# Optimization experiments

Measured on AMD Instinct MI355X. Metric: run time of the kernel, lower is better.

Reference implementation:

```python
import jax, jax.numpy as jnp
import numpy as np
import math

B, L, HID = 2, 2048, 1024
H, DK, RATIO, SHARED, TOPK = 4, 64, 4, 1, 2
EXP_V = 2
DV = DK * EXP_V
KEY_DIM = H * DK
VAL_DIM = KEY_DIM * EXP_V
HE = H * RATIO
KS = 4
EPS = 1e-5


def _silu(x):
    return x * jax.nn.sigmoid(x)


def _dwconv_causal(x, w):
    # x: (B, L, C), w: (C, KS); causal depthwise short conv
    xp = jnp.pad(x, ((0, 0), (KS - 1, 0), (0, 0))).transpose(0, 2, 1)
    y = jax.lax.conv_general_dilated(xp, w[:, None, :], (1,), 'VALID',
                                     feature_group_count=w.shape[0],
                                     dimension_numbers=('NCH', 'OIH', 'NCH'))
    return y.transpose(0, 2, 1)


def _l2norm(x):
    return x * jax.lax.rsqrt(jnp.sum(x * x, -1, keepdims=True) + 1e-6)


def _forward(hidden_states, Wq, Wk, Wv, Wb, Wa, Wg, Wo, conv_q, conv_k, conv_v,
             Wq_exp, Wk_exp, W_gate, A_log, dt_bias, norm_w):
    x = hidden_states
    q = _silu(_dwconv_causal(x @ Wq.T, conv_q)).reshape(B, L, H, DK)
    k = _silu(_dwconv_causal(x @ Wk.T, conv_k)).reshape(B, L, H, DK)
    v = _silu(_dwconv_causal(x @ Wv.T, conv_v)).reshape(B, L, H, DV)
    # per-head expert expansion -> (B,L,H,RATIO,DK)
    qe = jnp.einsum('blhd,hkd->blhk', q, Wq_exp).reshape(B, L, H, RATIO, DK)
    ke = jnp.einsum('blhd,hkd->blhk', k, Wk_exp).reshape(B, L, H, RATIO, DK)
    qe = _l2norm(qe) * (DK ** -0.5)
    ke = _l2norm(ke)
    # token-policy top-k routing over non-shared experts
    logits = jnp.einsum('blhd,nd->blhn', q, W_gate)
    scores = jax.nn.softmax(logits.astype(jnp.float32), axis=-1)
    tw, ti = jax.lax.top_k(scores, TOPK)
    tw = tw / jnp.sum(tw, -1, keepdims=True)
    full = jnp.sum(jax.nn.one_hot(ti + SHARED, RATIO, dtype=tw.dtype) * tw[..., None], axis=-2)
    full = full.at[..., :SHARED].set(1.0 / SHARED)
    w_r = (full / jnp.sum(full, -1, keepdims=True)).astype(x.dtype)  # (B,L,H,RATIO)
    mask = (w_r > 0).astype(x.dtype)
    beta = jax.nn.sigmoid(x @ Wb.T).reshape(B, L, H, RATIO) * mask
    g = -jnp.exp(A_log).reshape(H, RATIO) * jax.nn.softplus((x @ Wa.T) + dt_bias).reshape(B, L, H, RATIO)
    g = g * mask  # unrouted memories: exp(0)=1, no decay, no update
    # gated delta-rule recurrence over HE = H*RATIO memories
    qs = qe.reshape(B, L, HE, DK).transpose(1, 0, 2, 3)
    ks_ = ke.reshape(B, L, HE, DK).transpose(1, 0, 2, 3)
    vs = jnp.broadcast_to(v[:, :, :, None, :], (B, L, H, RATIO, DV)).reshape(B, L, HE, DV).transpose(1, 0, 2, 3)
    bs = beta.reshape(B, L, HE).transpose(1, 0, 2)
    gs = g.reshape(B, L, HE).transpose(1, 0, 2)

    def step(S, xs):
        qt, kt, vt, bt, gt = xs
        S = S * jnp.exp(gt)[..., None, None]
        kv = jnp.einsum('bhk,bhkv->bhv', kt, S)
        S = S + jnp.einsum('bhk,bhv->bhkv', kt, (vt - kv) * bt[..., None])
        return S, jnp.einsum('bhk,bhkv->bhv', qt, S)

    S0 = jnp.zeros((B, HE, DK, DV), x.dtype)
    _, o = jax.lax.scan(step, S0, (qs, ks_, vs, bs, gs))
    o = o.transpose(1, 0, 2, 3).reshape(B, L, H, RATIO, DV)
    o = jnp.einsum('blhe,blhev->blhv', w_r, o)
    # FusedRMSNormSwishGate + output projection
    gate = (x @ Wg.T).reshape(B, L, H, DV)
    o = o * jax.lax.rsqrt(jnp.mean(o * o, -1, keepdims=True) + EPS) * norm_w * _silu(gate)
    return o.reshape(B, L, VAL_DIM) @ Wo.T


def setup_inputs():
    keys = jax.random.split(jax.random.key(0), 18)
    n = lambda i, shp, sc=1.0: jax.random.normal(keys[i], shp, jnp.float32) * sc
    A = jax.random.uniform(keys[14], (HE,), jnp.float32, 1e-3, 16.0)
    dt = jnp.exp(jax.random.uniform(keys[15], (HE,), jnp.float32) * (math.log(0.1) - math.log(0.001)) + math.log(0.001))
    dt = jnp.clip(dt, 1e-4, None)
    return {
        'hidden_states': n(0, (B, L, HID)),
        'Wq': n(1, (KEY_DIM, HID), HID ** -0.5),
        'Wk': n(2, (KEY_DIM, HID), HID ** -0.5),
        'Wv': n(3, (VAL_DIM, HID), HID ** -0.5),
        'Wb': n(4, (HE, HID), HID ** -0.5),
        'Wa': n(5, (HE, HID), HID ** -0.5),
        'Wg': n(6, (VAL_DIM, HID), HID ** -0.5),
        'Wo': n(7, (HID, VAL_DIM), VAL_DIM ** -0.5),
        'conv_q': n(8, (KEY_DIM, KS), 0.5),
        'conv_k': n(9, (KEY_DIM, KS), 0.5),
        'conv_v': n(10, (VAL_DIM, KS), 0.5),
        'Wq_exp': n(11, (H, RATIO * DK, DK), DK ** -0.5),
        'Wk_exp': n(12, (H, RATIO * DK, DK), DK ** -0.5),
        'W_gate': n(13, (RATIO - SHARED, DK), DK ** -0.5),
        'A_log': jnp.log(A),
        'dt_bias': dt + jnp.log(-jnp.expm1(-dt)),
        'norm_w': jnp.ones((DV,), jnp.float32),
    }


def reference(hidden_states, Wq, Wk, Wv, Wb, Wa, Wg, Wo, conv_q, conv_k, conv_v,
              Wq_exp, Wk_exp, W_gate, A_log, dt_bias, norm_w):
    return _forward(hidden_states, Wq, Wk, Wv, Wb, Wa, Wg, Wo, conv_q, conv_k, conv_v,
                    Wq_exp, Wk_exp, W_gate, A_log, dt_bias, norm_w)
```

## Files before the change

### kernel.cpp

```cpp
#include <hip/hip_runtime.h>
#include <hip/hip_bf16.h>
#include <math.h>

#define B_    2
#define L_    2048
#define HID_  1024
#define H_    4
#define DK_   64
#define RATIO_ 4
#define HE_   16
#define DV_   128
#define T_    64
#define NC_   32
#define SPITCH 72
#define APITCH 68
#define NCAT  1408

typedef __attribute__((ext_vector_type(8))) short short8;
typedef __attribute__((ext_vector_type(4))) float f32x4;

__device__ __forceinline__ float sigmoidf_(float x){ return 1.f/(1.f+expf(-x)); }
__device__ __forceinline__ ushort f2bf(float x){
  __hip_bfloat16 h = __float2bfloat16(x);
  return *reinterpret_cast<ushort*>(&h);
}
__device__ __forceinline__ float bf2f(ushort u){
  union { uint32_t i; float f; } v; v.i = ((uint32_t)u) << 16; return v.f;
}
__device__ __forceinline__ void unpk8(uint4 w, float* f){
  f[0]=bf2f((ushort)(w.x&0xffff)); f[1]=bf2f((ushort)(w.x>>16));
  f[2]=bf2f((ushort)(w.y&0xffff)); f[3]=bf2f((ushort)(w.y>>16));
  f[4]=bf2f((ushort)(w.z&0xffff)); f[5]=bf2f((ushort)(w.z>>16));
  f[6]=bf2f((ushort)(w.w&0xffff)); f[7]=bf2f((ushort)(w.w>>16));
}

__global__ __launch_bounds__(256) void cast_bf16(const float* __restrict__ in,
                                                 ushort* __restrict__ out, int n)
{
  int i = blockIdx.x*256 + threadIdx.x;
  if (i < n) out[i] = f2bf(in[i]);
}

__global__ __launch_bounds__(256) void concat_wcat(const float* __restrict__ Wk,
    const float* __restrict__ Wv, const float* __restrict__ Wg,
    const float* __restrict__ Wb, const float* __restrict__ Wa,
    ushort* __restrict__ Wcat)
{
  int idx = blockIdx.x*256 + threadIdx.x;
  if (idx >= NCAT*1024) return;
  int r = idx >> 10, cc = idx & 1023;
  float v = 0.f;
  if      (r < 256)  v = Wk[(size_t)r*1024 + cc];
  else if (r < 768)  v = Wv[(size_t)(r-256)*1024 + cc];
  else if (r < 1280) v = Wg[(size_t)(r-768)*1024 + cc];
  else if (r < 1296) v = Wb[(size_t)(r-1280)*1024 + cc];
  else if (r < 1312) v = Wa[(size_t)(r-1296)*1024 + cc];
  Wcat[idx] = f2bf(v);
}

__global__ __launch_bounds__(256) void gemm_bf16(
    const ushort* __restrict__ A, int lda,
    const ushort* __restrict__ Bm, int ldb,
    float* __restrict__ C, int ldc, int K)
{
  __shared__ ushort As[128*32];
  __shared__ ushort Bs[128*32];
  const int tid  = threadIdx.x;
  const int wave = tid >> 6, lane = tid & 63;
  const int row0 = blockIdx.y*128, col0 = blockIdx.x*128;
  const int wr = (wave >> 1) * 64, wc = (wave & 1) * 64;
  const int frow = lane & 15;
  const int fko  = (lane >> 4) << 3;
  f32x4 acc[4][4];
  #pragma unroll
  for (int i=0;i<4;i++)
    #pragma unroll
    for (int j=0;j<4;j++) acc[i][j] = (f32x4){0.f,0.f,0.f,0.f};
  for (int k0 = 0; k0 < K; k0 += 32) {
    #pragma unroll
    for (int cc = 0; cc < 2; cc++) {
      int c  = wave*128 + cc*64 + lane;
      int r  = c >> 2;
      int ko = (c & 3) << 3;
      __builtin_amdgcn_global_load_lds(
        (const __attribute__((address_space(1))) void*)(A + (size_t)(row0+r)*lda + k0 + ko),
        (__attribute__((address_space(3))) void*)(As + (size_t)(wave*128 + cc*64)*8),
        16, 0, 0);
      __builtin_amdgcn_global_load_lds(
        (const __attribute__((address_space(1))) void*)(Bm + (size_t)(col0+r)*ldb + k0 + ko),
        (__attribute__((address_space(3))) void*)(Bs + (size_t)(wave*128 + cc*64)*8),
        16, 0, 0);
    }
    __syncthreads();
    short8 af[4], bfv[4];
    #pragma unroll
    for (int mi=0;mi<4;mi++)
      af[mi] = *reinterpret_cast<const short8*>(&As[(wr + mi*16 + frow)*32 + fko]);
    #pragma unroll
    for (int ni=0;ni<4;ni++)
      bfv[ni] = *reinterpret_cast<const short8*>(&Bs[(wc + ni*16 + frow)*32 + fko]);
    #pragma unroll
    for (int mi=0;mi<4;mi++)
      #pragma unroll
      for (int ni=0;ni<4;ni++)
        acc[mi][ni] = __builtin_amdgcn_mfma_f32_16x16x32_bf16(af[mi], bfv[ni], acc[mi][ni], 0, 0, 0);
    __syncthreads();
  }
  const int ocol = lane & 15;
  const int orow = (lane >> 4) << 2;
  #pragma unroll
  for (int mi=0;mi<4;mi++)
    #pragma unroll
    for (int ni=0;ni<4;ni++) {
      size_t base = (size_t)(row0 + wr + mi*16 + orow)*ldc + (col0 + wc + ni*16 + ocol);
      #pragma unroll
      for (int q=0;q<4;q++) C[base + (size_t)q*ldc] = acc[mi][ni][q];
    }
}

__global__ __launch_bounds__(256) void gemm_expand_bf16(
    const ushort* __restrict__ qc_bf, const ushort* __restrict__ kc_bf,
    const ushort* __restrict__ Wqeb, const ushort* __restrict__ Wkeb,
    ushort* __restrict__ qeb, ushort* __restrict__ keb)
{
  const int z = blockIdx.z;
  const int hh = z & 3;
  const ushort* A  = (z < 4 ? qc_bf : kc_bf) + hh*64;
  const ushort* Bm = (z < 4 ? Wqeb  : Wkeb ) + (size_t)hh*16384;
  ushort* C        = (z < 4 ? qeb   : keb  ) + hh*256;
  const int lda = 256, ldb = 64, ldc = 1024, K = 64;
  __shared__ ushort As[128*32];
  __shared__ ushort Bs[128*32];
  const int tid  = threadIdx.x;
  const int wave = tid >> 6, lane = tid & 63;
  const int row0 = blockIdx.y*128, col0 = blockIdx.x*128;
  const int wr = (wave >> 1) * 64, wc = (wave & 1) * 64;
  const int frow = lane & 15;
  const int fko  = (lane >> 4) << 3;
  f32x4 acc[4][4];
  #pragma unroll
  for (int i=0;i<4;i++)
    #pragma unroll
    for (int j=0;j<4;j++) acc[i][j] = (f32x4){0.f,0.f,0.f,0.f};
  for (int k0 = 0; k0 < K; k0 += 32) {
    #pragma unroll
    for (int cc = 0; cc < 2; cc++) {
      int c  = wave*128 + cc*64 + lane;
      int r  = c >> 2;
      int ko = (c & 3) << 3;
      __builtin_amdgcn_global_load_lds(
        (const __attribute__((address_space(1))) void*)(A + (size_t)(row0+r)*lda + k0 + ko),
        (__attribute__((address_space(3))) void*)(As + (size_t)(wave*128 + cc*64)*8),
        16, 0, 0);
      __builtin_amdgcn_global_load_lds(
        (const __attribute__((address_space(1))) void*)(Bm + (size_t)(col0+r)*ldb + k0 + ko),
        (__attribute__((address_space(3))) void*)(Bs + (size_t)(wave*128 + cc*64)*8),
        16, 0, 0);
    }
    __syncthreads();
    short8 af[4], bfv[4];
    #pragma unroll
    for (int mi=0;mi<4;mi++)
      af[mi] = *reinterpret_cast<const short8*>(&As[(wr + mi*16 + frow)*32 + fko]);
    #pragma unroll
    for (int ni=0;ni<4;ni++)
      bfv[ni] = *reinterpret_cast<const short8*>(&Bs[(wc + ni*16 + frow)*32 + fko]);
    #pragma unroll
    for (int mi=0;mi<4;mi++)
      #pragma unroll
      for (int ni=0;ni<4;ni++)
        acc[mi][ni] = __builtin_amdgcn_mfma_f32_16x16x32_bf16(af[mi], bfv[ni], acc[mi][ni], 0, 0, 0);
    __syncthreads();
  }
  const int ocol = lane & 15;
  const int orow = (lane >> 4) << 2;
  #pragma unroll
  for (int mi=0;mi<4;mi++)
    #pragma unroll
    for (int ni=0;ni<4;ni++) {
      size_t base = (size_t)(row0 + wr + mi*16 + orow)*ldc + (col0 + wc + ni*16 + ocol);
      #pragma unroll
      for (int q=0;q<4;q++) C[base + (size_t)q*ldc] = f2bf(acc[mi][ni][q]);
    }
}

__global__ __launch_bounds__(256) void gemm_f32_db(const float* __restrict__ A, int lda,
    const float* __restrict__ Bm, int ldb, float* __restrict__ C, int ldc,
    int M, int N, int K)
{
  __shared__ float As[2][32][64];
  __shared__ float Bs[2][32][64];
  const int tid = threadIdx.x;
  const int row0 = blockIdx.y * 64;
  const int col0 = blockIdx.x * 64;
  const int tx = tid & 15, ty = tid >> 4;
  const int r0s = tid >> 3;
  const int k4s = (tid & 7) << 2;
  float4 av0, av1, bv0, bv1;

  av0 = *(const float4*)&A[(size_t)(row0 + r0s)*lda + k4s];
  av1 = *(const float4*)&A[(size_t)(row0 + r0s + 32)*lda + k4s];
  bv0 = (col0 + r0s < N) ? *(const float4*)&Bm[(size_t)(col0 + r0s)*ldb + k4s] : make_float4(0,0,0,0);
  bv1 = (col0 + r0s + 32 < N) ? *(const float4*)&Bm[(size_t)(col0 + r0s + 32)*ldb + k4s] : make_float4(0,0,0,0);
  As[0][k4s+0][r0s] = av0.x; As[0][k4s+1][r0s] = av0.y; As[0][k4s+2][r0s] = av0.z; As[0][k4s+3][r0s] = av0.w;
  As[0][k4s+0][r0s+32] = av1.x; As[0][k4s+1][r0s+32] = av1.y; As[0][k4s+2][r0s+32] = av1.z; As[0][k4s+3][r0s+32] = av1.w;
  Bs[0][k4s+0][r0s] = bv0.x; Bs[0][k4s+1][r0s] = bv0.y; Bs[0][k4s+2][r0s] = bv0.z; Bs[0][k4s+3][r0s] = bv0.w;
  Bs[0][k4s+0][r0s+32] = bv1.x; Bs[0][k4s+1][r0s+32] = bv1.y; Bs[0][k4s+2][r0s+32] = bv1.z; Bs[0][k4s+3][r0s+32] = bv1.w;
  __syncthreads();

  float acc[4][4] = {};
  const int nt = K >> 5;
  for (int kt = 0; kt < nt; ++kt) {
    const int p = kt & 1;
    if (kt + 1 < nt) {
      int k0 = (kt+1) << 5;
      av0 = *(const float4*)&A[(size_t)(row0 + r0s)*lda + k0 + k4s];
      av1 = *(const float4*)&A[(size_t)(row0 + r0s + 32)*lda + k0 + k4s];
      bv0 = (col0 + r0s < N) ? *(const float4*)&Bm[(size_t)(col0 + r0s)*ldb + k0 + k4s] : make_float4(0,0,0,0);
      bv1 = (col0 + r0s + 32 < N) ? *(const float4*)&Bm[(size_t)(col0 + r0s + 32)*ldb + k0 + k4s] : make_float4(0,0,0,0);
    }
    #pragma unroll
    for (int kk = 0; kk < 32; kk++) {
      float4 a4 = *(const float4*)&As[p][kk][ty*4];
      float4 b4 = *(const float4*)&Bs[p][kk][tx*4];
      float a[4] = {a4.x,a4.y,a4.z,a4.w};
      float b[4] = {b4.x,b4.y,b4.z,b4.w};
      #pragma unroll
      for (int i=0;i<4;i++)
        #pragma unroll
        for (int j=0;j<4;j++) acc[i][j] += a[i]*b[j];
    }
    if (kt + 1 < nt) {
      const int q = p ^ 1;
      As[q][k4s+0][r0s] = av0.x; As[q][k4s+1][r0s] = av0.y; As[q][k4s+2][r0s] = av0.z; As[q][k4s+3][r0s] = av0.w;
      As[q][k4s+0][r0s+32] = av1.x; As[q][k4s+1][r0s+32] = av1.y; As[q][k4s+2][r0s+32] = av1.z; As[q][k4s+3][r0s+32] = av1.w;
      Bs[q][k4s+0][r0s] = bv0.x; Bs[q][k4s+1][r0s] = bv0.y; Bs[q][k4s+2][r0s] = bv0.z; Bs[q][k4s+3][r0s] = bv0.w;
      Bs[q][k4s+0][r0s+32] = bv1.x; Bs[q][k4s+1][r0s+32] = bv1.y; Bs[q][k4s+2][r0s+32] = bv1.z; Bs[q][k4s+3][r0s+32] = bv1.w;
    }
    __syncthreads();
  }
  #pragma unroll
  for (int i=0;i<4;i++) {
    int r = row0 + ty*4 + i;
    #pragma unroll
    for (int j=0;j<4;j++) {
      int cc = col0 + tx*4 + j;
      if (cc < N) C[(size_t)r*ldc + cc] = acc[i][j];
    }
  }
}

__global__ __launch_bounds__(256) void conv_silu(const float* __restrict__ in, int ild,
    const float* __restrict__ w, float* __restrict__ outf, ushort* __restrict__ outb,
    int C, int total)
{
  int n = blockIdx.x*256 + threadIdx.x;
  if (n >= total) return;
  int c = n % C;
  int t = (n / C) % L_;
  int b = n / (C*L_);
  float acc = 0.f;
  #pragma unroll
  for (int s = 0; s < 4; s++) {
    int tt = t - 3 + s;
    if (tt >= 0) acc += in[((size_t)b*L_ + tt)*ild + c] * w[c*4+s];
  }
  float y = acc * sigmoidf_(acc);
  if (outf) outf[n] = y;
  if (outb) outb[n] = f2bf(y);
}

__global__ __launch_bounds__(256) void routing(const float* __restrict__ qc,
    const float* __restrict__ kvgba, const float* __restrict__ Wg3,
    const float* __restrict__ A_log, const float* __restrict__ dt_bias,
    float* __restrict__ w_buf, float* __restrict__ bt_buf, float* __restrict__ g_buf)
{
  int n = blockIdx.x*256 + threadIdx.x;
  int h  = n & 3;
  int bl = n >> 2;
  const float* q = qc + (size_t)bl*256 + h*64;
  float l0=0.f, l1=0.f, l2=0.f;
  for (int d=0; d<64; d++) {
    float qd = q[d];
    l0 += qd*Wg3[d]; l1 += qd*Wg3[64+d]; l2 += qd*Wg3[128+d];
  }
  float mx = fmaxf(l0, fmaxf(l1, l2));
  float e0 = expf(l0-mx), e1 = expf(l1-mx), e2 = expf(l2-mx);
  float inv_s = 1.f/(e0+e1+e2);
  float p0 = e0*inv_s, p1 = e1*inv_s, p2 = e2*inv_s;
  int m1 = 0; float pm1 = p0;
  if (p1 > pm1) { m1 = 1; pm1 = p1; }
  if (p2 > pm1) { m1 = 2; pm1 = p2; }
  int ia = (m1==0) ? 1 : 0;
  int ib = (m1==2) ? 1 : 2;
  float pa = (m1==0) ? p1 : p0;
  float pb = (m1==2) ? p1 : p2;
  int   m2  = (pb > pa) ? ib : ia;
  float pm2 = (pb > pa) ? pb : pa;
  float inv_w = 1.f/(pm1 + pm2);
  float w1 = 0.5f*pm1*inv_w;
  float w2 = 0.5f*pm2*inv_w;
  #pragma unroll
  for (int r = 0; r < 4; r++) {
    float wr = (r==0) ? 0.5f : (((r-1)==m1) ? w1 : (((r-1)==m2) ? w2 : 0.f));
    int he = h*4 + r;
    size_t gi = (size_t)bl*16 + he;
    w_buf[gi] = wr;
    float mask = (wr > 0.f) ? 1.f : 0.f;
    bt_buf[gi] = mask * sigmoidf_(kvgba[(size_t)bl*NCAT + 1280 + he]);
    float av = kvgba[(size_t)bl*NCAT + 1296 + he] + dt_bias[he];
    float sp = fmaxf(av, 0.f) + log1pf(expf(-fabsf(av)));
    g_buf[gi] = -expf(A_log[he]) * sp * mask;
  }
}

__global__ __launch_bounds__(256) void l2norm_rows_bf(ushort* __restrict__ v, float scale)
{
  int row  = blockIdx.x*4 + (threadIdx.x >> 6);
  int lane = threadIdx.x & 63;
  size_t idx = (size_t)row*64 + lane;
  float x = bf2f(v[idx]);
  float ss = x*x;
  #pragma unroll
  for (int off = 32; off > 0; off >>= 1) ss += __shfl_xor(ss, off);
  v[idx] = f2bf(x * rsqrtf(ss + 1e-6f) * scale);
}

__device__ __forceinline__ f32x4 tile64(const ushort* Am, int r0,
                                        const ushort* Bm, int c0, int lane)
{
  f32x4 acc = {0.f,0.f,0.f,0.f};
  const int fr = lane & 15, fo = (lane >> 4) << 3;
  #pragma unroll
  for (int kk = 0; kk < 2; ++kk) {
    short8 a = *reinterpret_cast<const short8*>(&Am[(r0+fr)*SPITCH + fo + kk*32]);
    short8 b = *reinterpret_cast<const short8*>(&Bm[(c0+fr)*SPITCH + fo + kk*32]);
    acc = __builtin_amdgcn_mfma_f32_16x16x32_bf16(a, b, acc, 0, 0, 0);
  }
  return acc;
}

__global__ __launch_bounds__(256,2) void scan_chunk_mfma(
    const ushort* __restrict__ keb, const ushort* __restrict__ qeb,
    const ushort* __restrict__ vcb, const float* __restrict__ bt_buf,
    const float* __restrict__ g_buf, float* __restrict__ o_r,
    ushort* __restrict__ Qtb, ushort* __restrict__ Mcb, ushort* __restrict__ Bcb)
{
  __shared__ float smem[18496];
  ushort* Kbf = (ushort*)smem;
  ushort* Qbf = (ushort*)(smem + 2304);
  ushort* KTD = (ushort*)(smem + 4608);
  float*  Af  = smem + 6912;
  ushort* Pf  = (ushort*)(smem + 6912);
  ushort* UV  = (ushort*)(smem + 11264);
  float*  cgs = smem + 18176;
  float*  bts = cgs + 64;
  float*  bGs = bts + 64;
  float*  Ds  = bGs + 64;
  float*  gams= Ds + 64;

  const int id = blockIdx.x;
  const int c   = id >> 5;
  const int bhe = id & 31;
  const int b  = bhe >> 4;
  const int he = bhe & 15;
  const int h = he >> 2;
  const int tid = threadIdx.x;
  const int wave = tid >> 6, lane = tid & 63;
  const size_t l0 = (size_t)b*L_ + (size_t)c*T_;

  const int tr = tid >> 2;
  const int sg = tid & 3;
  uint32_t kwv[8], qwv[8];
  uint4 vw0, vw1, vw2, vw3;
  {
    const uint4* kp = (const uint4*)(keb + (l0+tr)*1024 + he*64 + sg*16);
    const uint4* qp = (const uint4*)(qeb + (l0+tr)*1024 + he*64 + sg*16);
    uint4 k0 = kp[0], k1 = kp[1], q0 = qp[0], q1 = qp[1];
    kwv[0]=k0.x; kwv[1]=k0.y; kwv[2]=k0.z; kwv[3]=k0.w;
    kwv[4]=k1.x; kwv[5]=k1.y; kwv[6]=k1.z; kwv[7]=k1.w;
    qwv[0]=q0.x; qwv[1]=q0.y; qwv[2]=q0.z; qwv[3]=q0.w;
    qwv[4]=q1.x; qwv[5]=q1.y; qwv[6]=q1.z; qwv[7]=q1.w;
    const uint4* vp = (const uint4*)(vcb + (l0+tr)*512 + h*128 + sg*32);
    vw0 = vp[0]; vw1 = vp[1]; vw2 = vp[2]; vw3 = vp[3];
  }
  if (tid < 64) {
    float g  = g_buf[(l0+tid)*HE_ + he];
    float bt = bt_buf[(l0+tid)*HE_ + he];
    float cg = g;
    #pragma unroll
    for (int off = 1; off < 64; off <<= 1) {
      float o = __shfl_up(cg, off);
      if (tid >= off) cg += o;
    }
    float cg63 = __shfl(cg, 63);
    cgs[tid] = cg; bts[tid] = bt;
    float gm = expf(cg);
    gams[tid] = gm; bGs[tid] = bt*gm; Ds[tid] = expf(cg63 - cg);
  }
  __syncthreads();
  {
    float Dt = Ds[tr];
    uint2* kdst = (uint2*)(Kbf + tr*SPITCH + sg*16);
    uint2* qdst = (uint2*)(Qbf + tr*SPITCH + sg*16);
    #pragma unroll
    for (int i=0;i<4;i++){
      kdst[i] = make_uint2(kwv[2*i], kwv[2*i+1]);
      qdst[i] = make_uint2(qwv[2*i], qwv[2*i+1]);
    }
    #pragma unroll
    for (int i=0;i<8;i++){
      ushort lo = (ushort)(kwv[i] & 0xffff), hi = (ushort)(kwv[i] >> 16);
      int d = sg*16 + 2*i;
      KTD[(d+0)*SPITCH + tr] = f2bf(bf2f(lo)*Dt);
      KTD[(d+1)*SPITCH + tr] = f2bf(bf2f(hi)*Dt);
    }
    uint4* vdst = (uint4*)(UV + tr*128 + sg*32);
    vdst[0] = vw0; vdst[1] = vw1; vdst[2] = vw2; vdst[3] = vw3;
  }
  __syncthreads();
  {
    const int r0 = wave*16;
    #pragma unroll
    for (int ct=0; ct<4; ++ct) {
      f32x4 acc = tile64(Kbf, r0, Kbf, ct*16, lane);
      int t = r0 + ((lane>>4)<<2);
      int s = ct*16 + (lane&15);
      #pragma unroll
      for (int q=0;q<4;q++){
        int tq = t + q;
        Af[tq*APITCH + s] = (s < tq) ? bts[tq]*expf(cgs[tq]-cgs[s])*acc[q] : 0.f;
      }
    }
  }
  __syncthreads();
  float u[64];
  if (tid < 192) {
    if (tid < 128) {
      const ushort* Vb = UV;
      #pragma unroll
      for (int s=0;s<64;++s) u[s] = bts[s]*bf2f(Vb[s*128 + tid]);
    } else {
      #pragma unroll
      for (int s=0;s<64;++s) u[s] = bGs[s]*bf2f(Kbf[s*SPITCH + (tid-128)]);
    }
  }
  __syncthreads();
  if (tid < 192) {
    #pragma unroll
    for (int t=1;t<64;++t) {
      const float4* Ar = (const float4*)(Af + t*APITCH);
      float p0=0.f,p1=0.f,p2=0.f,p3=0.f;
      #pragma unroll
      for (int s4=0; s4*4<t; ++s4) {
        float4 a = Ar[s4];
        p0 += a.x*u[s4*4+0]; p1 += a.y*u[s4*4+1];
        p2 += a.z*u[s4*4+2]; p3 += a.w*u[s4*4+3];
      }
      u[t] -= (p0+p1)+(p2+p3);
    }
    ushort* Ut = UV;
    uint4* dst = (uint4*)&Ut[tid*SPITCH];
    #pragma unroll
    for (int i=0;i<8;++i) {
      uint32_t w0 = ((uint32_t)f2bf(u[8*i+1])<<16) | f2bf(u[8*i+0]);
      uint32_t w1 = ((uint32_t)f2bf(u[8*i+3])<<16) | f2bf(u[8*i+2]);
      uint32_t w2 = ((uint32_t)f2bf(u[8*i+5])<<16) | f2bf(u[8*i+4]);
      uint32_t w3 = ((uint32_t)f2bf(u[8*i+7])<<16) | f2bf(u[8*i+6]);
      dst[i] = make_uint4(w0,w1,w2,w3);
    }
  }
  __syncthreads();
  {
    const int r0 = wave*16;
    f32x4 accs[4];
    #pragma unroll
    for (int ct=0; ct<4; ++ct) accs[ct] = tile64(Qbf, r0, Kbf, ct*16, lane);
    __syncthreads();
    #pragma unroll
    for (int ct=0; ct<4; ++ct) {
      int t = r0 + ((lane>>4)<<2);
      int s = ct*16 + (lane&15);
      #pragma unroll
      for (int q=0;q<4;q++){
        int tq = t + q;
        float val = (s <= tq) ? expf(cgs[tq]-cgs[s])*accs[ct][q] : 0.f;
        Pf[tq*SPITCH + s] = f2bf(val);
      }
    }
  }
  __syncthreads();
  {
    const int r0 = wave*16;
    const float gend = expf(cgs[63]);
    const ushort* Ut = UV;
    const ushort* UtK = UV + 128*SPITCH;
    const size_t bb = ((size_t)bhe*NC_ + c)*(size_t)(64*128);
    const size_t pb = ((size_t)bhe*NC_ + c)*(size_t)(64*64);
    #pragma unroll
    for (int jt=0; jt<8; ++jt) {
      f32x4 acc = tile64(Pf, r0, Ut, jt*16, lane);
      int t = r0 + ((lane>>4)<<2);
      int j = jt*16 + (lane&15);
      #pragma unroll
      for (int q=0;q<4;q++)
        o_r[((l0 + t + q)*HE_ + he)*DV_ + j] = acc[q];
    }
    #pragma unroll
    for (int jt=0; jt<8; ++jt) {
      f32x4 acc = tile64(KTD, r0, Ut, jt*16, lane);
      int i = r0 + ((lane>>4)<<2);
      int j = jt*16 + (lane&15);
      #pragma unroll
      for (int q=0;q<4;q++)
        Bcb[bb + (size_t)(i+q)*128 + j] = f2bf(acc[q]);
    }
    #pragma unroll
    for (int ct=0; ct<4; ++ct) {
      f32x4 acc = tile64(KTD, r0, UtK, ct*16, lane);
      int i = r0 + ((lane>>4)<<2);
      int m = ct*16 + (lane&15);
      #pragma unroll
      for (int q=0;q<4;q++){
        float val = -acc[q];
        int row = i + q;
        if (row == m) val += gend;
        int pc = (((m>>3)^(row&7))<<3) | (m&7);
        Mcb[pb + (size_t)row*64 + pc] = f2bf(val);
      }
    }
    #pragma unroll
    for (int ct=0; ct<4; ++ct) {
      f32x4 acc = tile64(Pf, r0, UtK, ct*16, lane);
      int t = r0 + ((lane>>4)<<2);
      int m = ct*16 + (lane&15);
      #pragma unroll
      for (int q=0;q<4;q++){
        int row = t + q;
        int pc = (((m>>3)^(row&7))<<3) | (m&7);
        Qtb[pb + (size_t)row*64 + pc] = f2bf(gams[row]*bf2f(Qbf[row*SPITCH + m]) - acc[q]);
      }
    }
  }
}

__device__ __forceinline__ void stage_qm(const ushort* __restrict__ src, ushort* dst,
                                         int wave, int lane)
{
  #pragma unroll
  for (int pass = 0; pass < 2; ++pass){
    int idx = pass*256 + wave*64 + lane;
    __builtin_amdgcn_global_load_lds(
      (const __attribute__((address_space(1))) void*)(src + (size_t)idx*8),
      (__attribute__((address_space(3))) void*)(dst + (size_t)idx*8), 16, 0, 0);
  }
}

__global__ __launch_bounds__(256) void compose_correct(
    const ushort* __restrict__ Mcb, const ushort* __restrict__ Bcb,
    const ushort* __restrict__ Qtb, float* __restrict__ o_r)
{
  __shared__ ushort Ql[2][4096];
  __shared__ ushort Ml[2][4096];
  __shared__ float SSl[1024];
  const int bhe = blockIdx.x;
  const int j0  = blockIdx.y * 16;
  const int b = bhe >> 4, he = bhe & 15;
  const int tid = threadIdx.x;
  const int wave = tid >> 6, lane = tid & 63;
  const int rw = tid >> 2;
  const int jg = tid & 3;
  const int rsw = rw & 7;

  for (int id = tid; id < 1024; id += 256) SSl[id] = 0.f;

  stage_qm(Mcb + (size_t)(bhe*NC_)*4096, Ml[0], wave, lane);
  float4 bcur;
  {
    uint2 bw = *(const uint2*)&Bcb[(size_t)(bhe*NC_)*8192 + rw*128 + j0 + jg*4];
    bcur = make_float4(bf2f((ushort)(bw.x&0xffff)), bf2f((ushort)(bw.x>>16)),
                       bf2f((ushort)(bw.y&0xffff)), bf2f((ushort)(bw.y>>16)));
  }
  __syncthreads();

  int p = 0;
  for (int c = 0; c < NC_; ++c){
    float4 bnext = make_float4(0.f,0.f,0.f,0.f);
    if (c+1 < NC_){
      stage_qm(Qtb + (size_t)(bhe*NC_ + c + 1)*4096, Ql[p^1], wave, lane);
      if (c+1 < NC_-1){
        stage_qm(Mcb + (size_t)(bhe*NC_ + c + 1)*4096, Ml[p^1], wave, lane);
        uint2 bw = *(const uint2*)&Bcb[(size_t)(bhe*NC_ + c + 1)*8192 + rw*128 + j0 + jg*4];
        bnext = make_float4(bf2f((ushort)(bw.x&0xffff)), bf2f((ushort)(bw.x>>16)),
                            bf2f((ushort)(bw.y&0xffff)), bf2f((ushort)(bw.y>>16)));
      }
    }
    const float4* SS4 = (const float4*)SSl;
    if (c > 0){
      float4 oa = make_float4(0.f,0.f,0.f,0.f);
      const ushort* Qr = Ql[p] + rw*64;
      #pragma unroll
      for (int gb = 0; gb < 8; ++gb){
        uint4 w = *(const uint4*)&Qr[(gb ^ rsw) << 3];
        float f[8]; unpk8(w, f);
        #pragma unroll
        for (int e = 0; e < 8; ++e){
          float4 s = SS4[(gb*8+e)*4 + jg];
          oa.x += f[e]*s.x; oa.y += f[e]*s.y; oa.z += f[e]*s.z; oa.w += f[e]*s.w;
        }
      }
      size_t oi = (((size_t)b*L_ + c*T_ + rw)*HE_ + he)*DV_ + j0 + jg*4;
      float4 o = *(float4*)&o_r[oi];
      o.x += oa.x; o.y += oa.y; o.z += oa.z; o.w += oa.w;
      *(float4*)&o_r[oi] = o;
    }
    float4 ns = bcur;
    if (c < NC_-1){
      const ushort* Mr = Ml[p] + rw*64;
      #pragma unroll
      for (int gb = 0; gb < 8; ++gb){
        uint4 w = *(const uint4*)&Mr[(gb ^ rsw) << 3];
        float f[8]; unpk8(w, f);
        #pragma unroll
        for (int e = 0; e < 8; ++e){
          float4 s = SS4[(gb*8+e)*4 + jg];
          ns.x += f[e]*s.x; ns.y += f[e]*s.y; ns.z += f[e]*s.z; ns.w += f[e]*s.w;
        }
      }
    }
    __syncthreads();
    if (c < NC_-1) *(float4*)&SSl[rw*16 + jg*4] = ns;
    __syncthreads();
    p ^= 1;
    bcur = bnext;
  }
}

__global__ __launch_bounds__(128) void combine(const float* __restrict__ o_r,
    const float* __restrict__ w_buf, const float* __restrict__ kvgba,
    const float* __restrict__ norm_w, ushort* __restrict__ o_fin)
{
  int n  = blockIdx.x;
  int h  = n & 3;
  int bl = n >> 2;
  int j  = threadIdx.x;
  size_t wb = (size_t)bl*16 + h*4;
  size_t ob = wb*128 + j;
  float oc = 0.f;
  #pragma unroll
  for (int r = 0; r < 4; r++) oc += w_buf[wb+r] * o_r[ob + (size_t)r*128];
  float ss = oc*oc;
  #pragma unroll
  for (int off = 32; off > 0; off >>= 1) ss += __shfl_xor(ss, off);
  __shared__ float red[2];
  if ((threadIdx.x & 63) == 0) red[threadIdx.x >> 6] = ss;
  __syncthreads();
  float mean = (red[0] + red[1]) * (1.f/128.f);
  float sc = rsqrtf(mean + 1e-5f);
  float gv = kvgba[(size_t)bl*NCAT + 768 + h*128 + j];
  o_fin[(size_t)bl*512 + h*128 + j] = f2bf(oc * sc * norm_w[j] * (gv * sigmoidf_(gv)));
}

extern "C" void kernel_launch(void* const* d_in, const int* in_sizes, int n_in,
                              void* d_out, int out_size, void* d_ws, size_t ws_size,
                              hipStream_t stream)
{
  (void)in_sizes; (void)n_in; (void)out_size; (void)ws_size;
  const float* x       = (const float*)d_in[0];
  const float* Wq      = (const float*)d_in[1];
  const float* Wk      = (const float*)d_in[2];
  const float* Wv      = (const float*)d_in[3];
  const float* Wb      = (const float*)d_in[4];
  const float* Wa      = (const float*)d_in[5];
  const float* Wg      = (const float*)d_in[6];
  const float* Wo      = (const float*)d_in[7];
  const float* conv_q  = (const float*)d_in[8];
  const float* conv_k  = (const float*)d_in[9];
  const float* conv_v  = (const float*)d_in[10];
  const float* Wq_exp  = (const float*)d_in[11];
  const float* Wk_exp  = (const float*)d_in[12];
  const float* W_gate  = (const float*)d_in[13];
  const float* A_log   = (const float*)d_in[14];
  const float* dt_bias = (const float*)d_in[15];
  const float* norm_w  = (const float*)d_in[16];
  float* out = (float*)d_out;

  const size_t BL = (size_t)B_*L_;
  float* p = (float*)d_ws;
  float* q_lin  = p; p += BL*256;
  float* kvgba  = p; p += BL*NCAT;
  float* q_conv = p; p += BL*256;
  float* w_buf  = p; p += BL*16;
  float* bt_buf = p; p += BL*16;
  float* g_buf  = p; p += BL*16;
  float* o_r    = p; p += BL*16*128;
  ushort* Mcb   = (ushort*)p; p += (size_t)B_*HE_*NC_*2048;
  ushort* Qtb   = (ushort*)p; p += (size_t)B_*HE_*NC_*2048;
  ushort* Bcb   = (ushort*)p; p += (size_t)B_*HE_*NC_*4096;
  ushort* v_convb=(ushort*)p; p += BL*256;
  ushort* xb    = (ushort*)p; p += BL*512;
  ushort* Wcat  = (ushort*)p; p += (NCAT*1024)/2;
  ushort* qc_bf = (ushort*)p; p += BL*128;
  ushort* kc_bf = (ushort*)p; p += BL*128;
  ushort* qeb   = (ushort*)p; p += BL*512;
  ushort* keb   = (ushort*)p; p += BL*512;
  ushort* Wqeb  = (ushort*)p; p += 32768;
  ushort* Wkeb  = (ushort*)p; p += 32768;
  ushort* Wob   = (ushort*)p; p += 262144;
  ushort* o_finb= (ushort*)p; p += BL*256;

  concat_wcat<<<dim3((NCAT*1024+255)/256), dim3(256), 0, stream>>>(Wk, Wv, Wg, Wb, Wa, Wcat);
  { int n = (int)(BL*1024); cast_bf16<<<dim3((n+255)/256), dim3(256), 0, stream>>>(x, xb, n); }
  { int n = 65536;  cast_bf16<<<dim3((n+255)/256), dim3(256), 0, stream>>>(Wq_exp, Wqeb, n); }
  { int n = 65536;  cast_bf16<<<dim3((n+255)/256), dim3(256), 0, stream>>>(Wk_exp, Wkeb, n); }
  { int n = 524288; cast_bf16<<<dim3((n+255)/256), dim3(256), 0, stream>>>(Wo, Wob, n); }

  gemm_f32_db<<<dim3(4, 64), dim3(256), 0, stream>>>(x, 1024, Wq, 1024, q_lin, 256, 4096, 256, 1024);
  gemm_bf16<<<dim3(NCAT/128, 32), dim3(256), 0, stream>>>(xb, 1024, Wcat, 1024, kvgba, NCAT, 1024);

  { int tot = B_*L_*256; conv_silu<<<dim3((tot+255)/256), dim3(256), 0, stream>>>(q_lin, 256, conv_q, q_conv, qc_bf, 256, tot); }
  { int tot = B_*L_*256; conv_silu<<<dim3((tot+255)/256), dim3(256), 0, stream>>>(kvgba, NCAT, conv_k, (float*)nullptr, kc_bf, 256, tot); }
  { int tot = B_*L_*512; conv_silu<<<dim3((tot+255)/256), dim3(256), 0, stream>>>(kvgba + 256, NCAT, conv_v, (float*)nullptr, v_convb, 512, tot); }

  routing<<<dim3(64), dim3(256), 0, stream>>>(q_conv, kvgba, W_gate, A_log, dt_bias,
                                              w_buf, bt_buf, g_buf);

  gemm_expand_bf16<<<dim3(2, 32, 8), dim3(256), 0, stream>>>(qc_bf, kc_bf, Wqeb, Wkeb, qeb, keb);

  l2norm_rows_bf<<<dim3(16384), dim3(256), 0, stream>>>(qeb, 0.125f);
  l2norm_rows_bf<<<dim3(16384), dim3(256), 0, stream>>>(keb, 1.0f);

  scan_chunk_mfma<<<dim3(NC_*HE_*B_), dim3(256), 0, stream>>>(keb, qeb, v_convb, bt_buf, g_buf,
                                                              o_r, Qtb, Mcb, Bcb);
  compose_correct<<<dim3(32, 8), dim3(256), 0, stream>>>(Mcb, Bcb, Qtb, o_r);
  combine<<<dim3(B_*L_*H_), dim3(128), 0, stream>>>(o_r, w_buf, kvgba, norm_w, o_finb);

  gemm_bf16<<<dim3(8, 32), dim3(256), 0, stream>>>(o_finb, 512, Wob, 512, out, 1024, 512);
}
```

Before: 360.9 us.

## Fuse L2 norm into scan, store outputs in bf16, transpose gate buffers

Drops the two separate l2norm kernels and computes each row's L2 normalisation inside scan_chunk_mfma, right after loading keys and queries. The intra-chunk output and the inter-chunk correction now go to two separate bf16 buffers instead of an fp32 read-modify-write of o_r. combine sums the two buffers. The g and beta buffers are stored transposed so the scan reads them contiguously, and the block index mapping is reordered so heads sharing inputs run on neighbouring blocks. The aim is to cut kernel launches and global memory traffic, at the cost of bf16 rounding on the partial outputs.

Result: no change. 358.1 us (-0.8%).

```diff
diff --git a/kernel.cpp b/kernel.cpp
--- a/kernel.cpp
+++ b/kernel.cpp
@@ -26,6 +26,9 @@
 }
 __device__ __forceinline__ float bf2f(ushort u){
   union { uint32_t i; float f; } v; v.i = ((uint32_t)u) << 16; return v.f;
+}
+__device__ __forceinline__ uint32_t pk2(float a, float b){
+  return ((uint32_t)f2bf(b) << 16) | f2bf(a);
 }
 __device__ __forceinline__ void unpk8(uint4 w, float* f){
   f[0]=bf2f((ushort)(w.x&0xffff)); f[1]=bf2f((ushort)(w.x>>16));
@@ -273,7 +276,7 @@
 __global__ __launch_bounds__(256) void routing(const float* __restrict__ qc,
     const float* __restrict__ kvgba, const float* __restrict__ Wg3,
     const float* __restrict__ A_log, const float* __restrict__ dt_bias,
-    float* __restrict__ w_buf, float* __restrict__ bt_buf, float* __restrict__ g_buf)
+    float* __restrict__ w_buf, float* __restrict__ bt_T, float* __restrict__ g_T)
 {
   int n = blockIdx.x*256 + threadIdx.x;
   int h  = n & 3;
@@ -304,26 +307,13 @@
   for (int r = 0; r < 4; r++) {
     float wr = (r==0) ? 0.5f : (((r-1)==m1) ? w1 : (((r-1)==m2) ? w2 : 0.f));
     int he = h*4 + r;
-    size_t gi = (size_t)bl*16 + he;
-    w_buf[gi] = wr;
+    w_buf[(size_t)bl*16 + he] = wr;
     float mask = (wr > 0.f) ? 1.f : 0.f;
-    bt_buf[gi] = mask * sigmoidf_(kvgba[(size_t)bl*NCAT + 1280 + he]);
+    bt_T[(size_t)he*4096 + bl] = mask * sigmoidf_(kvgba[(size_t)bl*NCAT + 1280 + he]);
     float av = kvgba[(size_t)bl*NCAT + 1296 + he] + dt_bias[he];
     float sp = fmaxf(av, 0.f) + log1pf(expf(-fabsf(av)));
-    g_buf[gi] = -expf(A_log[he]) * sp * mask;
-  }
-}
-
-__global__ __launch_bounds__(256) void l2norm_rows_bf(ushort* __restrict__ v, float scale)
-{
-  int row  = blockIdx.x*4 + (threadIdx.x >> 6);
-  int lane = threadIdx.x & 63;
-  size_t idx = (size_t)row*64 + lane;
-  float x = bf2f(v[idx]);
-  float ss = x*x;
-  #pragma unroll
-  for (int off = 32; off > 0; off >>= 1) ss += __shfl_xor(ss, off);
-  v[idx] = f2bf(x * rsqrtf(ss + 1e-6f) * scale);
+    g_T[(size_t)he*4096 + bl] = -expf(A_log[he]) * sp * mask;
+  }
 }
 
 __device__ __forceinline__ f32x4 tile64(const ushort* Am, int r0,
@@ -342,8 +332,8 @@
 
 __global__ __launch_bounds__(256,2) void scan_chunk_mfma(
     const ushort* __restrict__ keb, const ushort* __restrict__ qeb,
-    const ushort* __restrict__ vcb, const float* __restrict__ bt_buf,
-    const float* __restrict__ g_buf, float* __restrict__ o_r,
+    const ushort* __restrict__ vcb, const float* __restrict__ bt_T,
+    const float* __restrict__ g_T, ushort* __restrict__ o0b,
     ushort* __restrict__ Qtb, ushort* __restrict__ Mcb, ushort* __restrict__ Bcb)
 {
   __shared__ float smem[18496];
@@ -360,33 +350,42 @@
   float*  gams= Ds + 64;
 
   const int id = blockIdx.x;
-  const int c   = id >> 5;
-  const int bhe = id & 31;
-  const int b  = bhe >> 4;
-  const int he = bhe & 15;
-  const int h = he >> 2;
+  const int c  = id >> 5;
+  const int s  = id & 31;
+  const int h  = s & 3;
+  const int b  = (s >> 2) & 1;
+  const int r  = s >> 3;
+  const int he = h*4 + r;
+  const int bhe = b*HE_ + he;
   const int tid = threadIdx.x;
   const int wave = tid >> 6, lane = tid & 63;
   const size_t l0 = (size_t)b*L_ + (size_t)c*T_;
 
   const int tr = tid >> 2;
   const int sg = tid & 3;
-  uint32_t kwv[8], qwv[8];
+  float kf[16], qf[16];
   uint4 vw0, vw1, vw2, vw3;
+  float sk, sq;
   {
     const uint4* kp = (const uint4*)(keb + (l0+tr)*1024 + he*64 + sg*16);
     const uint4* qp = (const uint4*)(qeb + (l0+tr)*1024 + he*64 + sg*16);
-    uint4 k0 = kp[0], k1 = kp[1], q0 = qp[0], q1 = qp[1];
-    kwv[0]=k0.x; kwv[1]=k0.y; kwv[2]=k0.z; kwv[3]=k0.w;
-    kwv[4]=k1.x; kwv[5]=k1.y; kwv[6]=k1.z; kwv[7]=k1.w;
-    qwv[0]=q0.x; qwv[1]=q0.y; qwv[2]=q0.z; qwv[3]=q0.w;
-    qwv[4]=q1.x; qwv[5]=q1.y; qwv[6]=q1.z; qwv[7]=q1.w;
+    uint4 kv[2] = {kp[0], kp[1]};
+    uint4 qv[2] = {qp[0], qp[1]};
+    unpk8(kv[0], kf); unpk8(kv[1], kf+8);
+    unpk8(qv[0], qf); unpk8(qv[1], qf+8);
+    float ssk = 0.f, ssq = 0.f;
+    #pragma unroll
+    for (int i=0;i<16;i++){ ssk += kf[i]*kf[i]; ssq += qf[i]*qf[i]; }
+    ssk += __shfl_xor(ssk, 1); ssk += __shfl_xor(ssk, 2);
+    ssq += __shfl_xor(ssq, 1); ssq += __shfl_xor(ssq, 2);
+    sk = rsqrtf(ssk + 1e-6f);
+    sq = rsqrtf(ssq + 1e-6f) * 0.125f;
     const uint4* vp = (const uint4*)(vcb + (l0+tr)*512 + h*128 + sg*32);
     vw0 = vp[0]; vw1 = vp[1]; vw2 = vp[2]; vw3 = vp[3];
   }
   if (tid < 64) {
-    float g  = g_buf[(l0+tid)*HE_ + he];
-    float bt = bt_buf[(l0+tid)*HE_ + he];
+    float g  = g_T[(size_t)he*4096 + l0 + tid];
+    float bt = bt_T[(size_t)he*4096 + l0 + tid];
     float cg = g;
     #pragma unroll
     for (int off = 1; off < 64; off <<= 1) {
@@ -405,15 +404,14 @@
     uint2* qdst = (uint2*)(Qbf + tr*SPITCH + sg*16);
     #pragma unroll
     for (int i=0;i<4;i++){
-      kdst[i] = make_uint2(kwv[2*i], kwv[2*i+1]);
-      qdst[i] = make_uint2(qwv[2*i], qwv[2*i+1]);
-    }
-    #pragma unroll
-    for (int i=0;i<8;i++){
-      ushort lo = (ushort)(kwv[i] & 0xffff), hi = (ushort)(kwv[i] >> 16);
-      int d = sg*16 + 2*i;
-      KTD[(d+0)*SPITCH + tr] = f2bf(bf2f(lo)*Dt);
-      KTD[(d+1)*SPITCH + tr] = f2bf(bf2f(hi)*Dt);
+      kdst[i] = make_uint2(pk2(kf[4*i+0]*sk, kf[4*i+1]*sk), pk2(kf[4*i+2]*sk, kf[4*i+3]*sk));
+      qdst[i] = make_uint2(pk2(qf[4*i+0]*sq, qf[4*i+1]*sq), pk2(qf[4*i+2]*sq, qf[4*i+3]*sq));
+    }
+    float skD = sk*Dt;
+    #pragma unroll
+    for (int i=0;i<16;i++){
+      int d = sg*16 + i;
+      KTD[d*SPITCH + tr] = f2bf(kf[i]*skD);
     }
     uint4* vdst = (uint4*)(UV + tr*128 + sg*32);
     vdst[0] = vw0; vdst[1] = vw1; vdst[2] = vw2; vdst[3] = vw3;
@@ -425,11 +423,11 @@
     for (int ct=0; ct<4; ++ct) {
       f32x4 acc = tile64(Kbf, r0, Kbf, ct*16, lane);
       int t = r0 + ((lane>>4)<<2);
-      int s = ct*16 + (lane&15);
+      int ss = ct*16 + (lane&15);
       #pragma unroll
       for (int q=0;q<4;q++){
         int tq = t + q;
-        Af[tq*APITCH + s] = (s < tq) ? bts[tq]*expf(cgs[tq]-cgs[s])*acc[q] : 0.f;
+        Af[tq*APITCH + ss] = (ss < tq) ? bts[tq]*expf(cgs[tq]-cgs[ss])*acc[q] : 0.f;
       }
     }
   }
@@ -439,10 +437,10 @@
     if (tid < 128) {
       const ushort* Vb = UV;
       #pragma unroll
-      for (int s=0;s<64;++s) u[s] = bts[s]*bf2f(Vb[s*128 + tid]);
+      for (int ss=0;ss<64;++ss) u[ss] = bts[ss]*bf2f(Vb[ss*128 + tid]);
     } else {
       #pragma unroll
-      for (int s=0;s<64;++s) u[s] = bGs[s]*bf2f(Kbf[s*SPITCH + (tid-128)]);
+      for (int ss=0;ss<64;++ss) u[ss] = bGs[ss]*bf2f(Kbf[ss*SPITCH + (tid-128)]);
     }
   }
   __syncthreads();
@@ -462,13 +460,9 @@
     ushort* Ut = UV;
     uint4* dst = (uint4*)&Ut[tid*SPITCH];
     #pragma unroll
-    for (int i=0;i<8;++i) {
-      uint32_t w0 = ((uint32_t)f2bf(u[8*i+1])<<16) | f2bf(u[8*i+0]);
-      uint32_t w1 = ((uint32_t)f2bf(u[8*i+3])<<16) | f2bf(u[8*i+2]);
-      uint32_t w2 = ((uint32_t)f2bf(u[8*i+5])<<16) | f2bf(u[8*i+4]);
-      uint32_t w3 = ((uint32_t)f2bf(u[8*i+7])<<16) | f2bf(u[8*i+6]);
-      dst[i] = make_uint4(w0,w1,w2,w3);
-    }
+    for (int i=0;i<8;++i)
+      dst[i] = make_uint4(pk2(u[8*i+0],u[8*i+1]), pk2(u[8*i+2],u[8*i+3]),
+                          pk2(u[8*i+4],u[8*i+5]), pk2(u[8*i+6],u[8*i+7]));
   }
   __syncthreads();
   {
@@ -480,12 +474,12 @@
     #pragma unroll
     for (int ct=0; ct<4; ++ct) {
       int t = r0 + ((lane>>4)<<2);
-      int s = ct*16 + (lane&15);
+      int ss = ct*16 + (lane&15);
       #pragma unroll
       for (int q=0;q<4;q++){
         int tq = t + q;
-        float val = (s <= tq) ? expf(cgs[tq]-cgs[s])*accs[ct][q] : 0.f;
-        Pf[tq*SPITCH + s] = f2bf(val);
+        float val = (ss <= tq) ? expf(cgs[tq]-cgs[ss])*accs[ct][q] : 0.f;
+        Pf[tq*SPITCH + ss] = f2bf(val);
       }
     }
   }
@@ -504,7 +498,7 @@
       int j = jt*16 + (lane&15);
       #pragma unroll
       for (int q=0;q<4;q++)
-        o_r[((l0 + t + q)*HE_ + he)*DV_ + j] = acc[q];
+        o0b[((l0 + t + q)*HE_ + he)*DV_ + j] = f2bf(acc[q]);
     }
     #pragma unroll
     for (int jt=0; jt<8; ++jt) {
@@ -558,14 +552,18 @@
 
 __global__ __launch_bounds__(256) void compose_correct(
     const ushort* __restrict__ Mcb, const ushort* __restrict__ Bcb,
-    const ushort* __restrict__ Qtb, float* __restrict__ o_r)
+    const ushort* __restrict__ Qtb, ushort* __restrict__ o_corrb)
 {
   __shared__ ushort Ql[2][4096];
   __shared__ ushort Ml[2][4096];
   __shared__ float SSl[1024];
-  const int bhe = blockIdx.x;
+  const int s   = blockIdx.x;
+  const int h   = s & 3;
+  const int b   = (s >> 2) & 1;
+  const int r   = s >> 3;
+  const int he  = h*4 + r;
+  const int bhe = b*HE_ + he;
   const int j0  = blockIdx.y * 16;
-  const int b = bhe >> 4, he = bhe & 15;
   const int tid = threadIdx.x;
   const int wave = tid >> 6, lane = tid & 63;
   const int rw = tid >> 2;
@@ -596,8 +594,8 @@
       }
     }
     const float4* SS4 = (const float4*)SSl;
+    float4 oa = make_float4(0.f,0.f,0.f,0.f);
     if (c > 0){
-      float4 oa = make_float4(0.f,0.f,0.f,0.f);
       const ushort* Qr = Ql[p] + rw*64;
       #pragma unroll
       for (int gb = 0; gb < 8; ++gb){
@@ -605,14 +603,14 @@
         float f[8]; unpk8(w, f);
         #pragma unroll
         for (int e = 0; e < 8; ++e){
-          float4 s = SS4[(gb*8+e)*4 + jg];
-          oa.x += f[e]*s.x; oa.y += f[e]*s.y; oa.z += f[e]*s.z; oa.w += f[e]*s.w;
+          float4 sv = SS4[(gb*8+e)*4 + jg];
+          oa.x += f[e]*sv.x; oa.y += f[e]*sv.y; oa.z += f[e]*sv.z; oa.w += f[e]*sv.w;
         }
       }
+    }
+    {
       size_t oi = (((size_t)b*L_ + c*T_ + rw)*HE_ + he)*DV_ + j0 + jg*4;
-      float4 o = *(float4*)&o_r[oi];
-      o.x += oa.x; o.y += oa.y; o.z += oa.z; o.w += oa.w;
-      *(float4*)&o_r[oi] = o;
+      *(uint2*)&o_corrb[oi] = make_uint2(pk2(oa.x, oa.y), pk2(oa.z, oa.w));
     }
     float4 ns = bcur;
     if (c < NC_-1){
@@ -623,8 +621,8 @@
         float f[8]; unpk8(w, f);
         #pragma unroll
         for (int e = 0; e < 8; ++e){
-          float4 s = SS4[(gb*8+e)*4 + jg];
-          ns.x += f[e]*s.x; ns.y += f[e]*s.y; ns.z += f[e]*s.z; ns.w += f[e]*s.w;
+          float4 sv = SS4[(gb*8+e)*4 + jg];
+          ns.x += f[e]*sv.x; ns.y += f[e]*sv.y; ns.z += f[e]*sv.z; ns.w += f[e]*sv.w;
         }
       }
     }
@@ -636,9 +634,10 @@
   }
 }
 
-__global__ __launch_bounds__(128) void combine(const float* __restrict__ o_r,
-    const float* __restrict__ w_buf, const float* __restrict__ kvgba,
-    const float* __restrict__ norm_w, ushort* __restrict__ o_fin)
+__global__ __launch_bounds__(128) void combine(const ushort* __restrict__ o0b,
+    const ushort* __restrict__ o_corrb, const float* __restrict__ w_buf,
+    const float* __restrict__ kvgba, const float* __restrict__ norm_w,
+    ushort* __restrict__ o_fin)
 {
   int n  = blockIdx.x;
   int h  = n & 3;
@@ -648,7 +647,10 @@
   size_t ob = wb*128 + j;
   float oc = 0.f;
   #pragma unroll
-  for (int r = 0; r < 4; r++) oc += w_buf[wb+r] * o_r[ob + (size_t)r*128];
+  for (int r = 0; r < 4; r++){
+    size_t oi = ob + (size_t)r*128;
+    oc += w_buf[wb+r] * (bf2f(o0b[oi]) + bf2f(o_corrb[oi]));
+  }
   float ss = oc*oc;
   #pragma unroll
   for (int off = 32; off > 0; off >>= 1) ss += __shfl_xor(ss, off);
@@ -691,9 +693,10 @@
   float* kvgba  = p; p += BL*NCAT;
   float* q_conv = p; p += BL*256;
   float* w_buf  = p; p += BL*16;
-  float* bt_buf = p; p += BL*16;
-  float* g_buf  = p; p += BL*16;
-  float* o_r    = p; p += BL*16*128;
+  float* bt_T   = p; p += BL*16;
+  float* g_T    = p; p += BL*16;
+  ushort* o0b   = (ushort*)p; p += BL*16*64;
+  ushort* o_corrb=(ushort*)p; p += BL*16*64;
   ushort* Mcb   = (ushort*)p; p += (size_t)B_*HE_*NC_*2048;
   ushort* Qtb   = (ushort*)p; p += (size_t)B_*HE_*NC_*2048;
   ushort* Bcb   = (ushort*)p; p += (size_t)B_*HE_*NC_*4096;
@@ -723,17 +726,14 @@
   { int tot = B_*L_*512; conv_silu<<<dim3((tot+255)/256), dim3(256), 0, stream>>>(kvgba + 256, NCAT, conv_v, (float*)nullptr, v_convb, 512, tot); }
 
   routing<<<dim3(64), dim3(256), 0, stream>>>(q_conv, kvgba, W_gate, A_log, dt_bias,
-                                              w_buf, bt_buf, g_buf);
+                                              w_buf, bt_T, g_T);
 
   gemm_expand_bf16<<<dim3(2, 32, 8), dim3(256), 0, stream>>>(qc_bf, kc_bf, Wqeb, Wkeb, qeb, keb);
 
-  l2norm_rows_bf<<<dim3(16384), dim3(256), 0, stream>>>(qeb, 0.125f);
-  l2norm_rows_bf<<<dim3(16384), dim3(256), 0, stream>>>(keb, 1.0f);
-
-  scan_chunk_mfma<<<dim3(NC_*HE_*B_), dim3(256), 0, stream>>>(keb, qeb, v_convb, bt_buf, g_buf,
-                                                              o_r, Qtb, Mcb, Bcb);
-  compose_correct<<<dim3(32, 8), dim3(256), 0, stream>>>(Mcb, Bcb, Qtb, o_r);
-  combine<<<dim3(B_*L_*H_), dim3(128), 0, stream>>>(o_r, w_buf, kvgba, norm_w, o_finb);
+  scan_chunk_mfma<<<dim3(NC_*HE_*B_), dim3(256), 0, stream>>>(keb, qeb, v_convb, bt_T, g_T,
+                                                              o0b, Qtb, Mcb, Bcb);
+  compose_correct<<<dim3(32, 8), dim3(256), 0, stream>>>(Mcb, Bcb, Qtb, o_corrb);
+  combine<<<dim3(B_*L_*H_), dim3(128), 0, stream>>>(o0b, o_corrb, w_buf, kvgba, norm_w, o_finb);
 
   gemm_bf16<<<dim3(8, 32), dim3(256), 0, stream>>>(o_finb, 512, Wob, 512, out, 1024, 512);
 }
```
